# Performance work log

Measured on AMD Instinct MI355X. Metric: run time of the kernel, lower is better.

Reference implementation:

```python
import jax, jax.numpy as jnp
import numpy as np

B, L, D = 8, 2048, 1024
NH, M = 32, 16            # TTTConfig defaults: num_attention_heads=32, mini_batch_size=16
HD = D // NH              # 32
NM = L // M               # 128 mini-batches
DI = 2048                 # FFN hidden (configs.d_lower)
BASE_LR = 1.0
EPS = 1e-6


def setup_inputs() -> dict:
    key = jax.random.key(0)
    ks = jax.random.split(key, 12)
    n = lambda k, s, sc=0.02: jax.random.normal(k, s, jnp.float32) * sc
    return dict(
        enc_input=jax.random.normal(ks[0], (B, L, D), jnp.float32),
        ln0_g=jnp.ones((D,), jnp.float32), ln0_b=jnp.zeros((D,), jnp.float32),
        Wq=n(ks[1], (D, D)), Wk=n(ks[2], (D, D)), Wv=n(ks[3], (D, D)), Wo=n(ks[4], (D, D)),
        W1=n(ks[5], (NH, HD, HD)), b1=jnp.zeros((NH, 1, HD), jnp.float32),
        token_idx_delta=jnp.zeros((M,), jnp.float32),
        lr_w=n(ks[6], (NH, D)), lr_b=jnp.zeros((NH,), jnp.float32),
        ttt_ln_g=jnp.ones((NH, HD), jnp.float32), ttt_ln_b=jnp.zeros((NH, HD), jnp.float32),
        post_g=jnp.ones((D,), jnp.float32), post_b=jnp.zeros((D,), jnp.float32),
        ffn_g=jnp.ones((D,), jnp.float32), ffn_b=jnp.zeros((D,), jnp.float32),
        fw1=n(ks[7], (D, DI)), fb1=jnp.zeros((DI,), jnp.float32),
        fw2=n(ks[8], (DI, D)), fb2=jnp.zeros((D,), jnp.float32),
    )


def _layernorm(x, g, b):
    mu = x.mean(-1, keepdims=True)
    v = ((x - mu) ** 2).mean(-1, keepdims=True)
    return (x - mu) * jax.lax.rsqrt(v + EPS) * g + b


def _rope(x):
    # x: [B,NH,L,HD]; standard rotary embedding, theta=10000
    half = HD // 2
    inv = 1.0 / (10000.0 ** (jnp.arange(0, HD, 2, dtype=jnp.float32) / HD))
    pos = jnp.arange(L, dtype=jnp.float32)
    fr = pos[:, None] * inv[None, :]                    # [L, HD/2]
    emb = jnp.concatenate([fr, fr], -1)                 # [L, HD]
    cos, sin = jnp.cos(emb), jnp.sin(emb)
    rot = jnp.concatenate([-x[..., half:], x[..., :half]], -1)
    return x * cos + rot * sin


def reference(enc_input, ln0_g, ln0_b, Wq, Wk, Wv, Wo, W1, b1, token_idx_delta,
              lr_w, lr_b, ttt_ln_g, ttt_ln_b, post_g, post_b,
              ffn_g, ffn_b, fw1, fb1, fw2, fb2):
    residual = enc_input
    x = _layernorm(enc_input, ln0_g, ln0_b)

    def heads(t):  # [B,L,D] -> [B,NH,L,HD]
        return t.reshape(B, L, NH, HD).transpose(0, 2, 1, 3)

    XQ = _rope(heads(x @ Wq))
    XK = _rope(heads(x @ Wk))
    XV = heads(x @ Wv)

    # per-token learnable learning rates (sigmoid gate), token_idx schedule
    X_mb = x.reshape(B, NM, M, D)
    ttt_lr = jax.nn.sigmoid(jnp.einsum('bnkc,hc->bhnk', X_mb, lr_w) + lr_b[None, :, None, None])
    ttt_lr_eta = BASE_LR * ttt_lr / HD                               # [B,NH,NM,M]
    token_idx = jnp.clip(1.0 / jnp.arange(1, M + 1, dtype=jnp.float32) + token_idx_delta, 0.0, None)
    eta = token_idx[None, None, None, :, None] * ttt_lr_eta[:, :, :, None, :]  # [B,NH,NM,M,M]

    def to_scan(t):  # [B,NH,L,HD] -> [NM,B,NH,M,HD]
        return t.reshape(B, NH, NM, M, HD).transpose(2, 0, 1, 3, 4)

    xs = (to_scan(XQ), to_scan(XK), to_scan(XV), eta.transpose(2, 0, 1, 3, 4))

    lw = ttt_ln_g[:, None, :]   # [NH,1,HD]
    lb = ttt_ln_b[:, None, :]
    tril = jnp.tril(jnp.ones((M, M), jnp.float32))

    def ln_fwd(z):
        mu = z.mean(-1, keepdims=True)
        v = ((z - mu) ** 2).mean(-1, keepdims=True)
        return (z - mu) * jax.lax.rsqrt(v + EPS) * lw + lb

    def ln_l2_bwd(z, tgt):
        # gradient of 0.5*||LN(z)-tgt||^2 w.r.t. z (fused LN l2 backward)
        mu = z.mean(-1, keepdims=True)
        v = ((z - mu) ** 2).mean(-1, keepdims=True)
        std = jnp.sqrt(v + EPS)
        xhat = (z - mu) / std
        gxh = (xhat * lw + lb - tgt) * lw
        return (HD * gxh - gxh.sum(-1, keepdims=True)
                - xhat * (gxh * xhat).sum(-1, keepdims=True)) / (HD * std)

    W1_0 = jnp.broadcast_to(W1[None], (B, NH, HD, HD))
    b1_0 = jnp.broadcast_to(b1[None], (B, NH, 1, HD))

    def step(carry, inp):
        W, bvec = carry
        q, k, v_, e = inp                                    # [B,NH,M,HD], e: [B,NH,M,M]
        Z1 = k @ W + bvec
        grad = ln_l2_bwd(Z1, v_ - k)                         # [B,NH,M,HD]
        Attn1 = tril * (q @ k.transpose(0, 1, 3, 2))         # causal dual-form attention
        b_bar = bvec - (tril * e) @ grad
        Z1_bar = q @ W - (e * Attn1) @ grad + b_bar
        last_e = e[:, :, -1, :, None]                        # [B,NH,M,1]
        W_new = W - (last_e * k).transpose(0, 1, 3, 2) @ grad
        b_new = bvec - (last_e * grad).sum(-2, keepdims=True)
        return (W_new, b_new), q + ln_fwd(Z1_bar)

    _, outs = jax.lax.scan(step, (W1_0, b1_0), xs)           # [NM,B,NH,M,HD]
    out = outs.transpose(1, 0, 3, 2, 4).reshape(B, L, D)     # -> [B,L,D]
    out = _layernorm(out, post_g, post_b) @ Wo               # post_norm + o_proj
    out = out + residual                                     # dropout = identity (eval)

    # PositionWiseFeedForward (pre-LN, residual)
    r2 = out
    h = _layernorm(out, ffn_g, ffn_b)
    h = jax.nn.relu(h @ fw1 + fb1) @ fw2 + fb2
    return h + r2
```

## Files before the change

kernel.cpp:

```cpp
#include <hip/hip_runtime.h>
#include <hip/hip_bf16.h>
#include <stdint.h>

#define B_   8
#define L_   2048
#define D_   1024
#define NH_  32
#define M_   16
#define NM_  128
#define HD_  32
#define DI_  2048
#define BL_  16384
#define EPS_ 1e-6f

typedef __attribute__((ext_vector_type(8))) short  s16x8;
typedef __attribute__((ext_vector_type(4))) short  s16x4;
typedef __attribute__((ext_vector_type(8))) __bf16 bf16x8;
typedef __attribute__((ext_vector_type(4))) float  f32x4;
typedef __attribute__((ext_vector_type(4))) unsigned u32x4;

__device__ __forceinline__ float bf2f(short s){
  unsigned u = ((unsigned)(unsigned short)s) << 16;
  return __builtin_bit_cast(float, u);
}
__device__ __forceinline__ short f2bf(float f){
  unsigned u = __builtin_bit_cast(unsigned, f);
  u = u + 0x7FFFu + ((u >> 16) & 1u);
  return (short)(u >> 16);
}
__device__ __forceinline__ unsigned cvtpk(float lo, float hi){
  unsigned r;
  asm("v_cvt_pk_bf16_f32 %0, %1, %2" : "=v"(r) : "v"(lo), "v"(hi));
  return r;
}
template<int N>
__device__ __forceinline__ float ror_add(float v){
  const int y = __builtin_amdgcn_update_dpp(
      0, __builtin_bit_cast(int, v), 0x120 + N, 0xF, 0xF, true);
  return v + __builtin_bit_cast(float, y);
}
__device__ __forceinline__ float rsum16d(float v){
  v = ror_add<1>(v); v = ror_add<2>(v); v = ror_add<4>(v); v = ror_add<8>(v);
  return v;
}
__device__ __forceinline__ void wgbar(){
  asm volatile("s_waitcnt lgkmcnt(0)" ::: "memory");
  __builtin_amdgcn_s_barrier();
  __builtin_amdgcn_sched_barrier(0);
}
__device__ __forceinline__ void gl16(const void* g, void* l){
  __builtin_amdgcn_global_load_lds(
      (const __attribute__((address_space(1))) void*)g,
      (__attribute__((address_space(3))) void*)l, 16, 0, 0);
}

__global__ __launch_bounds__(256) void transpose_cast(
    const float* __restrict__ in, short* __restrict__ out, int R, int Cc)
{
  __shared__ float t[32][33];
  const int lx = threadIdx.x & 31, ly = threadIdx.x >> 5;
  const int r0 = blockIdx.y * 32, c0 = blockIdx.x * 32;
  #pragma unroll
  for (int s = 0; s < 4; ++s){
    const int r = ly + s*8;
    t[r][lx] = in[(size_t)(r0 + r)*Cc + c0 + lx];
  }
  __syncthreads();
  #pragma unroll
  for (int s = 0; s < 4; ++s){
    const int r = ly + s*8;
    out[(size_t)(c0 + r)*R + r0 + lx] = f2bf(t[lx][r]);
  }
}

struct TC4 { const float *s0,*s1,*s2,*s3; short *d0,*d1,*d2,*d3; };
__global__ __launch_bounds__(256) void transpose_cast4(TC4 p)
{
  __shared__ float t[32][33];
  const int z = blockIdx.z;
  const float* in = (z==0)?p.s0:(z==1)?p.s1:(z==2)?p.s2:p.s3;
  short* out      = (z==0)?p.d0:(z==1)?p.d1:(z==2)?p.d2:p.d3;
  const int lx = threadIdx.x & 31, ly = threadIdx.x >> 5;
  const int r0 = blockIdx.y * 32, c0 = blockIdx.x * 32;
  #pragma unroll
  for (int s = 0; s < 4; ++s){
    const int r = ly + s*8;
    t[r][lx] = in[(size_t)(r0 + r)*1024 + c0 + lx];
  }
  __syncthreads();
  #pragma unroll
  for (int s = 0; s < 4; ++s){
    const int r = ly + s*8;
    out[(size_t)(c0 + r)*1024 + r0 + lx] = f2bf(t[lx][r]);
  }
}

__global__ __launch_bounds__(256) void misc_prep(
    const float* __restrict__ lr_w, short* __restrict__ lrwb,
    float* __restrict__ ct, float* __restrict__ st)
{
  const int idx = blockIdx.x*256 + threadIdx.x;
  if (idx < NH_*D_){
    lrwb[idx] = f2bf(lr_w[idx]);
  } else {
    const int k = idx - NH_*D_;
    const int l = k >> 4, j = k & 15;
    const float inv = powf(10000.f, -(float)j * (1.f/16.f));
    const float fr  = (float)l * inv;
    ct[k] = cosf(fr);
    st[k] = sinf(fr);
  }
}

__global__ __launch_bounds__(256) void ln_rows(
    const float* __restrict__ in, const float* __restrict__ g,
    const float* __restrict__ bta, short* __restrict__ out)
{
  const int row = blockIdx.x, tid = threadIdx.x;
  const float4 v = ((const float4*)(in + (size_t)row*D_))[tid];
  float s  = v.x + v.y + v.z + v.w;
  float s2 = v.x*v.x + v.y*v.y + v.z*v.z + v.w*v.w;
  #pragma unroll
  for (int m = 1; m < 64; m <<= 1){ s += __shfl_xor(s, m); s2 += __shfl_xor(s2, m); }
  __shared__ float rs[4], rq[4];
  if ((tid & 63) == 0){ rs[tid>>6] = s; rq[tid>>6] = s2; }
  __syncthreads();
  s  = rs[0] + rs[1] + rs[2] + rs[3];
  s2 = rq[0] + rq[1] + rq[2] + rq[3];
  const float mu   = s  * (1.f/D_);
  const float var  = s2 * (1.f/D_) - mu*mu;
  const float rstd = rsqrtf(var + EPS_);
  const float4 gg = ((const float4*)g)[tid];
  const float4 bb = ((const float4*)bta)[tid];
  s16x4 o;
  o[0] = f2bf((v.x - mu)*rstd*gg.x + bb.x);
  o[1] = f2bf((v.y - mu)*rstd*gg.y + bb.y);
  o[2] = f2bf((v.z - mu)*rstd*gg.z + bb.z);
  o[3] = f2bf((v.w - mu)*rstd*gg.w + bb.w);
  ((s16x4*)(out + (size_t)row*D_))[tid] = o;
}

__global__ __launch_bounds__(256) void ln_rows_bf(
    const short* __restrict__ in, const float* __restrict__ g,
    const float* __restrict__ bta, short* __restrict__ out)
{
  const int row = blockIdx.x, tid = threadIdx.x;
  const s16x4 v4 = ((const s16x4*)(in + (size_t)row*D_))[tid];
  float v[4];
  #pragma unroll
  for (int e = 0; e < 4; ++e) v[e] = bf2f(v4[e]);
  float s  = v[0]+v[1]+v[2]+v[3];
  float s2 = v[0]*v[0]+v[1]*v[1]+v[2]*v[2]+v[3]*v[3];
  #pragma unroll
  for (int m = 1; m < 64; m <<= 1){ s += __shfl_xor(s, m); s2 += __shfl_xor(s2, m); }
  __shared__ float rs[4], rq[4];
  if ((tid & 63) == 0){ rs[tid>>6] = s; rq[tid>>6] = s2; }
  __syncthreads();
  s  = rs[0] + rs[1] + rs[2] + rs[3];
  s2 = rq[0] + rq[1] + rq[2] + rq[3];
  const float mu   = s  * (1.f/D_);
  const float var  = s2 * (1.f/D_) - mu*mu;
  const float rstd = rsqrtf(var + EPS_);
  const float4 gg = ((const float4*)g)[tid];
  const float4 bb = ((const float4*)bta)[tid];
  s16x4 o;
  #pragma unroll
  for (int e = 0; e < 4; ++e){
    const float gv = (e==0)?gg.x:(e==1)?gg.y:(e==2)?gg.z:gg.w;
    const float bv = (e==0)?bb.x:(e==1)?bb.y:(e==2)?bb.z:bb.w;
    o[e] = f2bf((v[e] - mu)*rstd*gv + bv);
  }
  ((s16x4*)(out + (size_t)row*D_))[tid] = o;
}

template<int ACT, int OUTBF, int BIAS, int RES, int RESB, int QKVOUT>
__global__ __launch_bounds__(512, 2) void gemm256(
    const short* __restrict__ A, const short* __restrict__ Bt,
    const float* __restrict__ bias, const float* __restrict__ res,
    const short* __restrict__ resb,
    float* __restrict__ Cf, short* __restrict__ Cb,
    const float* __restrict__ ct, const float* __restrict__ st,
    int Mr, int N, int K)
{
  __shared__ __align__(16) short As[4][8192];
  __shared__ __align__(16) short Bs[4][8192];
  const int tid  = threadIdx.x;
  const int lane = tid & 63, wid = tid >> 6;
  const int wr = wid >> 2, wc = wid & 3;
  const int nwg = gridDim.x * gridDim.y;
  const int wg  = blockIdx.y * gridDim.x + blockIdx.x;
  const int swz = (wg & 7) * (nwg >> 3) + (wg >> 3);
  const int bx  = swz % gridDim.x, by = swz / gridDim.x;
  const int row0 = by * 256, col0 = bx * 256;

  f32x4 acc[8][4] = {};

  const int kswz = (((tid & 3) ^ ((tid >> 3) & 3)) << 3);
  const short* gAb = A  + (size_t)(row0 + (tid >> 2)) * K + kswz;
  const short* gBb = Bt + (size_t)(col0 + (tid >> 2)) * K + kswz;
  short* lAb = &As[0][0] + tid*8;
  short* lBb = &Bs[0][0] + tid*8;

  auto stage = [&](int bt2, int t2){
    const size_t kb = (size_t)t2 * 32;
    gl16(gAb + kb,                   lAb + bt2*8192);
    gl16(gAb + kb + 128*(size_t)K,   lAb + bt2*8192 + 4096);
    gl16(gBb + kb,                   lBb + bt2*8192);
    gl16(gBb + kb + 128*(size_t)K,   lBb + bt2*8192 + 4096);
  };

  const int fr = lane & 15;
  const int k0 = (((lane >> 4) ^ ((lane >> 1) & 3)) << 3);

  const int nK = K >> 5;
  stage(0, 0); stage(1, 1); stage(2, 2);
  asm volatile("s_waitcnt vmcnt(8)" ::: "memory");
  __builtin_amdgcn_s_barrier();

  for (int kt = 0; kt < nK; ++kt){
    const int bt = kt & 3;
    const short* Ab = &As[0][0] + bt*8192 + wr*4096;
    const short* Bb = &Bs[0][0] + bt*8192 + (wc >> 1)*4096 + (wc & 1)*2048;
    bf16x8 af[8], bfv[4];
    #pragma unroll
    for (int m = 0; m < 8; ++m)
      af[m] = *(const bf16x8*)(Ab + (m*16 + fr)*32 + k0);
    #pragma unroll
    for (int n = 0; n < 4; ++n)
      bfv[n] = *(const bf16x8*)(Bb + (n*16 + fr)*32 + k0);
    if (kt + 3 < nK) stage((kt + 3) & 3, kt + 3);
    __builtin_amdgcn_s_setprio(1);
    #pragma unroll
    for (int m = 0; m < 8; ++m)
      #pragma unroll
      for (int n = 0; n < 4; ++n)
        acc[m][n] = __builtin_amdgcn_mfma_f32_16x16x32_bf16(af[m], bfv[n], acc[m][n], 0,0,0);
    __builtin_amdgcn_s_setprio(0);
    if (kt + 3 < nK)      asm volatile("s_waitcnt vmcnt(8)" ::: "memory");
    else if (kt + 2 < nK) asm volatile("s_waitcnt vmcnt(4)" ::: "memory");
    else if (kt + 1 < nK) asm volatile("s_waitcnt vmcnt(0)" ::: "memory");
    __builtin_amdgcn_s_barrier();
  }

  const int cr = (lane >> 4) * 4, cc = lane & 15;
  if (QKVOUT){
    const int part = col0 >> 10;
    #pragma unroll
    for (int m = 0; m < 8; ++m){
      const int gr0 = row0 + wr*128 + m*16 + cr;
      const int bidx = gr0 >> 11, l0 = gr0 & (L_-1);
      const int nn = l0 >> 4;
      if (part < 2){
        #pragma unroll
        for (int np = 0; np < 2; ++np){
          const int gc = col0 + wc*64 + np*32 + cc;
          const int hh = (gc & 1023) >> 5;
          short* tile = Cb + ((size_t)(bidx*NH_ + hh)*NM_ + nn)*2048;
          s16x4 r0v, r1v;
          #pragma unroll
          for (int r = 0; r < 4; ++r){
            const int l = l0 + r;
            const float cv = ct[l*16 + cc], sv = st[l*16 + cc];
            const float x0 = acc[m][np*2][r], x1 = acc[m][np*2+1][r];
            const short q0 = f2bf(x0*cv - x1*sv);
            const short q1 = f2bf(x1*cv + x0*sv);
            tile[part*512 + (cr + r)*32 + cc]      = q0;
            tile[part*512 + (cr + r)*32 + cc + 16] = q1;
            r0v[r] = q0; r1v[r] = q1;
          }
          if (part == 1){
            *(s16x4*)(tile + 1024 + cc*16 + cr)      = r0v;
            *(s16x4*)(tile + 1024 + (cc+16)*16 + cr) = r1v;
          }
        }
      } else {
        #pragma unroll
        for (int n = 0; n < 4; ++n){
          const int gc = col0 + wc*64 + n*16 + cc;
          const int hh = (gc & 1023) >> 5, dd = gc & 31;
          short* tile = Cb + ((size_t)(bidx*NH_ + hh)*NM_ + nn)*2048;
          s16x4 p;
          #pragma unroll
          for (int r = 0; r < 4; ++r) p[r] = f2bf(acc[m][n][r]);
          *(s16x4*)(tile + 1536 + dd*16 + cr) = p;
        }
      }
    }
    return;
  }
  #pragma unroll
  for (int m = 0; m < 8; ++m){
    #pragma unroll
    for (int n = 0; n < 4; ++n){
      const int gc = col0 + wc*64 + n*16 + cc;
      float bv = 0.f;
      if (BIAS) bv = bias[gc];
      #pragma unroll
      for (int r = 0; r < 4; ++r){
        const int gr = row0 + wr*128 + m*16 + cr + r;
        float v = acc[m][n][r] + bv;
        if (RES)  v += res[(size_t)gr*N + gc];
        if (RESB) v += bf2f(resb[(size_t)gr*N + gc]);
        if (ACT == 1) v = fmaxf(v, 0.f);
        if (OUTBF) Cb[(size_t)gr*N + gc] = f2bf(v);
        else       Cf[(size_t)gr*N + gc] = v;
      }
    }
  }
}

__global__ __launch_bounds__(256) void eta_kernel(
    const short* __restrict__ xb, const short* __restrict__ lrwb,
    const float* __restrict__ lr_b, float* __restrict__ eta)
{
  __shared__ __align__(16) short wl[NH_*1032];
  const int tid = threadIdx.x;
  const int lane = tid & 63, wv = tid >> 6;
  const int li = lane & 15, lh = lane >> 4;
  #pragma unroll
  for (int s = 0; s < 16; ++s){
    const int e = tid + 256*s;
    const int hrow = e >> 7, c = (e & 127) * 8;
    *(s16x8*)(wl + hrow*1032 + c) = ((const s16x8*)lrwb)[e];
  }
  __syncthreads();

  const int t0 = (blockIdx.x*4 + wv) * 16;
  const short* xrow = xb + (size_t)(t0 + li)*1024 + 8*lh;
  const short* w0p = wl + li*1032 + 8*lh;
  const short* w1p = wl + (16 + li)*1032 + 8*lh;
  f32x4 acc0 = {}, acc1 = {};
  #pragma unroll 4
  for (int s = 0; s < 32; ++s){
    const bf16x8 a  = *(const bf16x8*)(xrow + s*32);
    const bf16x8 b0 = *(const bf16x8*)(w0p + s*32);
    const bf16x8 b1 = *(const bf16x8*)(w1p + s*32);
    acc0 = __builtin_amdgcn_mfma_f32_16x16x32_bf16(a, b0, acc0, 0,0,0);
    acc1 = __builtin_amdgcn_mfma_f32_16x16x32_bf16(a, b1, acc1, 0,0,0);
  }
  const int t = t0 + 4*lh;
  const int bidx = t >> 11, l = t & (L_-1), n = l >> 4, im = l & 15;
  float* e0 = eta + ((size_t)(bidx*NH_ + li)*NM_ + n)*M_ + im;
  float* e1 = eta + ((size_t)(bidx*NH_ + 16 + li)*NM_ + n)*M_ + im;
  const float lb0 = lr_b[li], lb1 = lr_b[16 + li];
  #pragma unroll
  for (int r = 0; r < 4; ++r){
    e0[r] = 1.f/(1.f + __expf(-(acc0[r] + lb0))) * (1.f/32.f);
    e1[r] = 1.f/(1.f + __expf(-(acc1[r] + lb1))) * (1.f/32.f);
  }
}

__global__ __launch_bounds__(192) void scan_kernel(
    const short* __restrict__ Q5, const float* __restrict__ eta,
    const float* __restrict__ W1, const float* __restrict__ b1,
    const float* __restrict__ tdelta, const float* __restrict__ lng,
    const float* __restrict__ lnb, short* __restrict__ out)
{
  const int bh = blockIdx.x;
  const int h = bh & 31, b = bh >> 5;
  const int lane = threadIdx.x & 63;
  const int wv = threadIdx.x >> 6;
  const int li = lane & 15, lh = lane >> 4;

  __shared__ __align__(16) short WTl[2][32*40];
  __shared__ __align__(16) short GTl[2][32*24];
  __shared__ float BBl[2][2][16];
  __shared__ __align__(16) float AT[16*20];
  __shared__ __align__(16) short QLl[2][16*40];

  const short* chain = Q5 + (size_t)bh * (NM_*2048);
  const float* ech   = eta + (size_t)bh * (NM_*16);

  float lw[2], lbv[2];
  #pragma unroll
  for (int hh = 0; hh < 2; ++hh){
    lw[hh]  = lng[h*32 + 16*hh + li];
    lbv[hh] = lnb[h*32 + 16*hh + li];
  }

  if (wv == 0){
    f32x4 Wq[2][2];
    #pragma unroll
    for (int rb = 0; rb < 2; ++rb)
      #pragma unroll
      for (int cb = 0; cb < 2; ++cb)
        #pragma unroll
        for (int r = 0; r < 4; ++r)
          Wq[rb][cb][r] = W1[h*1024 + (16*rb + 4*lh + r)*32 + 16*cb + li];
    float bb[2];
    bb[0] = b1[h*32 + li];  bb[1] = b1[h*32 + 16 + li];
    const float lef = fmaxf(1.f/16.f + tdelta[15], 0.f);

    auto writeWT = [&](int sl){
      #pragma unroll
      for (int cb = 0; cb < 2; ++cb)
        #pragma unroll
        for (int rb = 0; rb < 2; ++rb){
          const unsigned p0 = cvtpk(Wq[rb][cb][0], Wq[rb][cb][1]);
          const unsigned p1 = cvtpk(Wq[rb][cb][2], Wq[rb][cb][3]);
          *(uint64_t*)(&WTl[sl][0] + (16*cb + li)*40 + 16*rb + 4*lh) =
              ((uint64_t)p1 << 32) | p0;
        }
    };
    auto readWf = [&](int sl, bf16x8* Wf){
      Wf[0] = *(const bf16x8*)(&WTl[sl][0] + li*40 + 8*lh);
      Wf[1] = *(const bf16x8*)(&WTl[sl][0] + (16 + li)*40 + 8*lh);
    };

    writeWT(0);
    if (lh == 0){ BBl[0][0][li] = bb[0]; BBl[0][1][li] = bb[1]; }
    bf16x8 Wf[2];
    readWf(0, Wf);

    struct P0 { s16x8 kA, kTq0, kTq1; s16x4 kTe0, kTe1, vTe0, vTe1;
                f32x4 lr0, lr1, lr2, lr3; };
    auto ld0 = [&](int n) -> P0 {
      const short* t = chain + (size_t)n*2048;
      const float* e = ech + n*16;
      P0 p;
      p.kA   = *(const s16x8*)(t + 512 + li*32 + 8*lh);
      p.kTq0 = *(const s16x8*)(t + 1024 + li*16 + 8*(lh & 1));
      p.kTq1 = *(const s16x8*)(t + 1024 + (16 + li)*16 + 8*(lh & 1));
      p.kTe0 = *(const s16x4*)(t + 1024 + li*16 + 4*lh);
      p.kTe1 = *(const s16x4*)(t + 1024 + (16 + li)*16 + 4*lh);
      p.vTe0 = *(const s16x4*)(t + 1536 + li*16 + 4*lh);
      p.vTe1 = *(const s16x4*)(t + 1536 + (16 + li)*16 + 4*lh);
      p.lr0 = *(const f32x4*)(e);     p.lr1 = *(const f32x4*)(e + 4);
      p.lr2 = *(const f32x4*)(e + 8); p.lr3 = *(const f32x4*)(e + 12);
      return p;
    };

    P0 cur = ld0(0);
    wgbar();

    const int gcol = (8*lh) & 15;
    #pragma unroll 1
    for (int p = 0; p <= NM_; ++p){
      if (p < NM_){
        const int n = p;
        const int sl = n & 1;
        P0 nxt = ld0(n + 1 < NM_ ? n + 1 : NM_ - 1);
        const bf16x8 kAf = __builtin_bit_cast(bf16x8, cur.kA);

        f32x4 zac[2];
        #pragma unroll
        for (int hh = 0; hh < 2; ++hh){
          f32x4 c0; c0[0]=bb[hh]; c0[1]=bb[hh]; c0[2]=bb[hh]; c0[3]=bb[hh];
          zac[hh] = __builtin_amdgcn_mfma_f32_16x16x32_bf16(kAf, Wf[hh], c0, 0,0,0);
        }

        float xh[2][4], grad[2][4], rstdv[4];
        #pragma unroll
        for (int r = 0; r < 4; ++r){
          float s  = rsum16d(zac[0][r] + zac[1][r]);
          float q2 = rsum16d(zac[0][r]*zac[0][r] + zac[1][r]*zac[1][r]);
          const float mu  = s * (1.f/32.f);
          const float var = q2 * (1.f/32.f) - mu*mu;
          const float rstd = rsqrtf(var + EPS_);
          rstdv[r] = rstd;
          xh[0][r] = (zac[0][r] - mu) * rstd;
          xh[1][r] = (zac[1][r] - mu) * rstd;
        }
        #pragma unroll
        for (int r = 0; r < 4; ++r){
          const float t0 = bf2f(cur.vTe0[r]) - bf2f(cur.kTe0[r]);
          const float t1 = bf2f(cur.vTe1[r]) - bf2f(cur.kTe1[r]);
          const float g0 = (xh[0][r]*lw[0] + lbv[0] - t0)*lw[0];
          const float g1 = (xh[1][r]*lw[1] + lbv[1] - t1)*lw[1];
          const float sg  = rsum16d(g0 + g1);
          const float sgx = rsum16d(g0*xh[0][r] + g1*xh[1][r]);
          const float f = rstdv[r] * (1.f/32.f);
          grad[0][r] = (32.f*g0 - sg - xh[0][r]*sgx) * f;
          grad[1][r] = (32.f*g1 - sg - xh[1][r]*sgx) * f;
        }

        #pragma unroll
        for (int hh = 0; hh < 2; ++hh){
          const unsigned p0 = cvtpk(grad[hh][0], grad[hh][1]);
          const unsigned p1 = cvtpk(grad[hh][2], grad[hh][3]);
          *(uint64_t*)(&GTl[sl][0] + (16*hh + li)*24 + 4*lh) =
              ((uint64_t)p1 << 32) | p0;
        }
        bf16x8 gf[2];
        gf[0] = *(const bf16x8*)(&GTl[sl][0] + li*24 + gcol);
        gf[1] = *(const bf16x8*)(&GTl[sl][0] + (16 + li)*24 + gcol);

        const f32x4 plA = (lh & 1) ? cur.lr2 : cur.lr0;
        const f32x4 plB = (lh & 1) ? cur.lr3 : cur.lr1;
        #pragma unroll
        for (int rb = 0; rb < 2; ++rb){
          const s16x8 kq = rb ? cur.kTq1 : cur.kTq0;
          float av8[8];
          #pragma unroll
          for (int jj = 0; jj < 8; ++jj){
            const float lrv = (jj < 4) ? plA[jj] : plB[jj - 4];
            av8[jj] = (lh < 2) ? -lef * lrv * bf2f(kq[jj]) : 0.f;
          }
          u32x4 auv;
          auv[0] = cvtpk(av8[0], av8[1]); auv[1] = cvtpk(av8[2], av8[3]);
          auv[2] = cvtpk(av8[4], av8[5]); auv[3] = cvtpk(av8[6], av8[7]);
          const bf16x8 af = __builtin_bit_cast(bf16x8, auv);
          #pragma unroll
          for (int cb = 0; cb < 2; ++cb)
            Wq[rb][cb] = __builtin_amdgcn_mfma_f32_16x16x32_bf16(af, gf[cb], Wq[rb][cb], 0,0,0);
        }

        writeWT(sl ^ 1);
        readWf(sl ^ 1, Wf);

        f32x4 lrq;
        { const f32x4 t0 = (lh & 1) ? cur.lr1 : cur.lr0;
          const f32x4 t1 = (lh & 1) ? cur.lr3 : cur.lr2;
          lrq = (lh & 2) ? t1 : t0; }
        #pragma unroll
        for (int hh = 0; hh < 2; ++hh){
          float t = 0.f;
          #pragma unroll
          for (int r = 0; r < 4; ++r) t += lrq[r]*grad[hh][r];
          t += __shfl_xor(t, 16); t += __shfl_xor(t, 32);
          bb[hh] -= lef * t;
        }
        if (lh == 0){ BBl[sl ^ 1][0][li] = bb[0]; BBl[sl ^ 1][1][li] = bb[1]; }
        cur = nxt;
      }
      wgbar();
    }
  } else {
    const int par = wv - 1;
    const float tok_i = fmaxf(1.f/(float)(li+1) + tdelta[li], 0.f);
    short* outp = out + (size_t)b*L_*D_ + h*32;
    const int gcol = (8*lh) & 15;

    struct P1 { s16x8 qA, kA; f32x4 lr0, lr1, lr2, lr3; };
    auto ld1 = [&](int n) -> P1 {
      const short* t = chain + (size_t)n*2048;
      const float* e = ech + n*16;
      P1 p;
      p.qA = *(const s16x8*)(t + li*32 + 8*lh);
      p.kA = *(const s16x8*)(t + 512 + li*32 + 8*lh);
      p.lr0 = *(const f32x4*)(e);     p.lr1 = *(const f32x4*)(e + 4);
      p.lr2 = *(const f32x4*)(e + 8); p.lr3 = *(const f32x4*)(e + 12);
      return p;
    };

    auto outln = [&](int n, const f32x4* yac){
      #pragma unroll
      for (int r = 0; r < 4; ++r){
        const float s  = rsum16d(yac[0][r] + yac[1][r]);
        const float q2 = rsum16d(yac[0][r]*yac[0][r] + yac[1][r]*yac[1][r]);
        const float mu   = s * (1.f/32.f);
        const float var  = q2 * (1.f/32.f) - mu*mu;
        const float rstd = rsqrtf(var + EPS_);
        const int row = 4*lh + r;
        #pragma unroll
        for (int hh = 0; hh < 2; ++hh){
          const float qv = bf2f(QLl[n & 1][row*40 + 16*hh + li]);
          const float o  = qv + (yac[hh][r] - mu)*rstd*lw[hh] + lbv[hh];
          outp[(size_t)(n*16 + row)*D_ + 16*hh + li] = f2bf(o);
        }
      }
    };

    P1 cur = ld1(par);
    wgbar();

    f32x4 ycur[2] = {};
    bf16x8 pCur = {};
    #pragma unroll 1
    for (int p = 0; p <= NM_; ++p){
      if (p >= 1 && ((p - 1) & 1) == par){
        const int m = p - 1;
        const int sl = m & 1;
        bf16x8 gf0 = *(const bf16x8*)(&GTl[sl][0] + li*24 + gcol);
        bf16x8 gf1 = *(const bf16x8*)(&GTl[sl][0] + (16 + li)*24 + gcol);
        ycur[0] = __builtin_amdgcn_mfma_f32_16x16x32_bf16(pCur, gf0, ycur[0], 0,0,0);
        ycur[1] = __builtin_amdgcn_mfma_f32_16x16x32_bf16(pCur, gf1, ycur[1], 0,0,0);
        outln(m, ycur);
      }
      if (p < NM_ && (p & 1) == par){
        const int sl = p & 1;
        bf16x8 Wf0 = *(const bf16x8*)(&WTl[sl][0] + li*40 + 8*lh);
        bf16x8 Wf1 = *(const bf16x8*)(&WTl[sl][0] + (16 + li)*40 + 8*lh);
        const float bb0 = BBl[sl][0][li];
        const float bb1 = BBl[sl][1][li];

        P1 nxt = ld1(p + 2 < NM_ ? p + 2 : p);
        const bf16x8 qAf = __builtin_bit_cast(bf16x8, cur.qA);
        const bf16x8 kAf = __builtin_bit_cast(bf16x8, cur.kA);

        *(s16x8*)(&QLl[sl][0] + li*40 + 8*lh) = cur.qA;

        f32x4 aac = {};
        aac = __builtin_amdgcn_mfma_f32_16x16x32_bf16(qAf, kAf, aac, 0,0,0);
        #pragma unroll
        for (int r = 0; r < 4; ++r)
          AT[(4*lh + r)*20 + li] = aac[r];

        f32x4 arA = {}, arB = {};
        if (lh < 2){
          arA = *(const f32x4*)(AT + li*20 + 8*lh);
          arB = *(const f32x4*)(AT + li*20 + 8*lh + 4);
        }
        const f32x4 plA = (lh & 1) ? cur.lr2 : cur.lr0;
        const f32x4 plB = (lh & 1) ? cur.lr3 : cur.lr1;
        float pv[8];
        #pragma unroll
        for (int jj = 0; jj < 8; ++jj){
          const float av  = (jj < 4) ? arA[jj] : arB[jj - 4];
          const float lrv = (jj < 4) ? plA[jj] : plB[jj - 4];
          const bool ok = (lh < 2) && (8*lh + jj <= li);
          pv[jj] = ok ? -tok_i * lrv * (1.f + av) : 0.f;
        }
        u32x4 ppv;
        ppv[0] = cvtpk(pv[0], pv[1]); ppv[1] = cvtpk(pv[2], pv[3]);
        ppv[2] = cvtpk(pv[4], pv[5]); ppv[3] = cvtpk(pv[6], pv[7]);
        pCur = __builtin_bit_cast(bf16x8, ppv);

        { f32x4 c0; c0[0]=bb0; c0[1]=bb0; c0[2]=bb0; c0[3]=bb0;
          ycur[0] = __builtin_amdgcn_mfma_f32_16x16x32_bf16(qAf, Wf0, c0, 0,0,0); }
        { f32x4 c0; c0[0]=bb1; c0[1]=bb1; c0[2]=bb1; c0[3]=bb1;
          ycur[1] = __builtin_amdgcn_mfma_f32_16x16x32_bf16(qAf, Wf1, c0, 0,0,0); }

        cur = nxt;
      }
      wgbar();
    }
  }
}

extern "C" void kernel_launch(void* const* d_in, const int* in_sizes, int n_in,
                              void* d_out, int out_size, void* d_ws, size_t ws_size,
                              hipStream_t stream)
{
  const float* enc    = (const float*)d_in[0];
  const float* ln0_g  = (const float*)d_in[1];
  const float* ln0_b  = (const float*)d_in[2];
  const float* Wq     = (const float*)d_in[3];
  const float* Wk     = (const float*)d_in[4];
  const float* Wv     = (const float*)d_in[5];
  const float* Wo     = (const float*)d_in[6];
  const float* W1     = (const float*)d_in[7];
  const float* b1     = (const float*)d_in[8];
  const float* tdelta = (const float*)d_in[9];
  const float* lr_w   = (const float*)d_in[10];
  const float* lr_b   = (const float*)d_in[11];
  const float* ttt_g  = (const float*)d_in[12];
  const float* ttt_b  = (const float*)d_in[13];
  const float* post_g = (const float*)d_in[14];
  const float* post_b = (const float*)d_in[15];
  const float* ffn_g  = (const float*)d_in[16];
  const float* ffn_b  = (const float*)d_in[17];
  const float* fw1    = (const float*)d_in[18];
  const float* fb1    = (const float*)d_in[19];
  const float* fw2    = (const float*)d_in[20];
  const float* fb2    = (const float*)d_in[21];

  char* ws = (char*)d_ws;
  short* Q5    = (short*)(ws + 0);
  short* XB    = (short*)(ws + 134217728);
  short* SCANB = (short*)(ws + 134217728);
  short* WQKVT = (short*)(ws + 167772160);
  short* WOT   = (short*)(ws + 174063616);
  short* FW1T  = (short*)(ws + 176160768);
  short* FW2T  = (short*)(ws + 180355072);
  short* LRWB  = (short*)(ws + 184549376);
  float* CT    = (float*)(ws + 184614912);
  float* ST    = (float*)(ws + 184745984);
  float* ETA   = (float*)(ws + 184877056);
  short* YB    = (short*)(ws + 0);
  short* HB    = (short*)(ws + 33554432);
  short* T1    = (short*)(ws + 67108864);
  short* R2B   = (short*)(ws + 134217728);
  float* R2    = (float*)d_out;

  dim3 b256(256), b512(512);
  TC4 tc;
  tc.s0 = Wq; tc.s1 = Wk; tc.s2 = Wv; tc.s3 = Wo;
  tc.d0 = WQKVT; tc.d1 = WQKVT + 1048576; tc.d2 = WQKVT + 2097152; tc.d3 = WOT;
  transpose_cast4<<<dim3(32,32,4), b256, 0, stream>>>(tc);
  transpose_cast<<<dim3(64,32), b256, 0, stream>>>(fw1, FW1T, D_, DI_);
  transpose_cast<<<dim3(32,64), b256, 0, stream>>>(fw2, FW2T, DI_, D_);
  misc_prep<<<dim3(256), b256, 0, stream>>>(lr_w, LRWB, CT, ST);

  ln_rows<<<BL_, b256, 0, stream>>>(enc, ln0_g, ln0_b, XB);
  gemm256<0,0,0,0,0,1><<<dim3(12,64), b512, 0, stream>>>(XB, WQKVT, nullptr, nullptr, nullptr,
                                                         nullptr, Q5, CT, ST, BL_, 3072, D_);
  eta_kernel<<<dim3(256), b256, 0, stream>>>(XB, LRWB, lr_b, ETA);
  scan_kernel<<<dim3(256), dim3(192), 0, stream>>>(Q5, ETA, W1, b1, tdelta,
                                                   ttt_g, ttt_b, SCANB);
  ln_rows_bf<<<BL_, b256, 0, stream>>>(SCANB, post_g, post_b, YB);
  gemm256<0,1,0,1,0,0><<<dim3(4,64), b512, 0, stream>>>(YB, WOT, nullptr, enc, nullptr,
                                                        nullptr, R2B, nullptr, nullptr, BL_, D_, D_);
  ln_rows_bf<<<BL_, b256, 0, stream>>>(R2B, ffn_g, ffn_b, HB);
  gemm256<1,1,1,0,0,0><<<dim3(8,64), b512, 0, stream>>>(HB, FW1T, fb1, nullptr, nullptr,
                                                        nullptr, T1, nullptr, nullptr, BL_, DI_, D_);
  gemm256<0,0,1,0,1,0><<<dim3(4,64), b512, 0, stream>>>(T1, FW2T, fb2, nullptr, R2B,
                                                        R2, nullptr, nullptr, nullptr, BL_, D_, DI_);
}
```

Before: 504.8 us.

## Use 16x16x16 MFMA with register-resident operands to drop LDS transposes in scan

The weight update and the output correction now use 16x16x16 bf16 MFMAs, called through inline asm, whose K=16 operand layout matches the accumulator layout already held in registers. Gradients are packed straight from registers into a lane-indexed LDS buffer, replacing the transposed GTl layout. The attention matrix is computed transposed so each lane already holds its P row, which removes the AT LDS round trip and the kTq loads. The goal is to shorten the serial per-mini-batch critical path by removing LDS writes, reads and barriers, at the cost of fixed s_nop padding and asm volatile blocks the compiler cannot schedule around.

```diff
diff --git a/kernel.cpp b/kernel.cpp
--- a/kernel.cpp
+++ b/kernel.cpp
@@ -18,6 +18,7 @@
 typedef __attribute__((ext_vector_type(8))) __bf16 bf16x8;
 typedef __attribute__((ext_vector_type(4))) float  f32x4;
 typedef __attribute__((ext_vector_type(4))) unsigned u32x4;
+typedef __attribute__((ext_vector_type(2))) unsigned u32x2;
 
 __device__ __forceinline__ float bf2f(short s){
   unsigned u = ((unsigned)(unsigned short)s) << 16;
@@ -32,6 +33,16 @@
   unsigned r;
   asm("v_cvt_pk_bf16_f32 %0, %1, %2" : "=v"(r) : "v"(lo), "v"(hi));
   return r;
+}
+__device__ __forceinline__ void mfma16x2(s16x4 a, s16x4 b0, s16x4 b1,
+                                         f32x4& c0, f32x4& c1){
+  asm volatile(
+      "s_nop 1\n\t"
+      "v_mfma_f32_16x16x16_bf16 %0, %2, %3, %0\n\t"
+      "v_mfma_f32_16x16x16_bf16 %1, %2, %4, %1\n\t"
+      "s_nop 7\n\t"
+      "s_nop 3"
+      : "+v"(c0), "+v"(c1) : "v"(a), "v"(b0), "v"(b1));
 }
 template<int N>
 __device__ __forceinline__ float ror_add(float v){
@@ -363,9 +374,8 @@
   const int li = lane & 15, lh = lane >> 4;
 
   __shared__ __align__(16) short WTl[2][32*40];
-  __shared__ __align__(16) short GTl[2][32*24];
+  __shared__ __align__(16) unsigned PGl[2][256];
   __shared__ float BBl[2][2][16];
-  __shared__ __align__(16) float AT[16*20];
   __shared__ __align__(16) short QLl[2][16*40];
 
   const short* chain = Q5 + (size_t)bh * (NM_*2048);
@@ -412,15 +422,13 @@
     bf16x8 Wf[2];
     readWf(0, Wf);
 
-    struct P0 { s16x8 kA, kTq0, kTq1; s16x4 kTe0, kTe1, vTe0, vTe1;
+    struct P0 { s16x8 kA; s16x4 kTe0, kTe1, vTe0, vTe1;
                 f32x4 lr0, lr1, lr2, lr3; };
     auto ld0 = [&](int n) -> P0 {
       const short* t = chain + (size_t)n*2048;
       const float* e = ech + n*16;
       P0 p;
       p.kA   = *(const s16x8*)(t + 512 + li*32 + 8*lh);
-      p.kTq0 = *(const s16x8*)(t + 1024 + li*16 + 8*(lh & 1));
-      p.kTq1 = *(const s16x8*)(t + 1024 + (16 + li)*16 + 8*(lh & 1));
       p.kTe0 = *(const s16x4*)(t + 1024 + li*16 + 4*lh);
       p.kTe1 = *(const s16x4*)(t + 1024 + (16 + li)*16 + 4*lh);
       p.vTe0 = *(const s16x4*)(t + 1536 + li*16 + 4*lh);
@@ -433,7 +441,6 @@
     P0 cur = ld0(0);
     wgbar();
 
-    const int gcol = (8*lh) & 15;
     #pragma unroll 1
     for (int p = 0; p <= NM_; ++p){
       if (p < NM_){
@@ -474,44 +481,35 @@
           grad[1][r] = (32.f*g1 - sg - xh[1][r]*sgx) * f;
         }
 
-        #pragma unroll
-        for (int hh = 0; hh < 2; ++hh){
-          const unsigned p0 = cvtpk(grad[hh][0], grad[hh][1]);
-          const unsigned p1 = cvtpk(grad[hh][2], grad[hh][3]);
-          *(uint64_t*)(&GTl[sl][0] + (16*hh + li)*24 + 4*lh) =
-              ((uint64_t)p1 << 32) | p0;
-        }
-        bf16x8 gf[2];
-        gf[0] = *(const bf16x8*)(&GTl[sl][0] + li*24 + gcol);
-        gf[1] = *(const bf16x8*)(&GTl[sl][0] + (16 + li)*24 + gcol);
-
-        const f32x4 plA = (lh & 1) ? cur.lr2 : cur.lr0;
-        const f32x4 plB = (lh & 1) ? cur.lr3 : cur.lr1;
-        #pragma unroll
-        for (int rb = 0; rb < 2; ++rb){
-          const s16x8 kq = rb ? cur.kTq1 : cur.kTq0;
-          float av8[8];
-          #pragma unroll
-          for (int jj = 0; jj < 8; ++jj){
-            const float lrv = (jj < 4) ? plA[jj] : plB[jj - 4];
-            av8[jj] = (lh < 2) ? -lef * lrv * bf2f(kq[jj]) : 0.f;
-          }
-          u32x4 auv;
-          auv[0] = cvtpk(av8[0], av8[1]); auv[1] = cvtpk(av8[2], av8[3]);
-          auv[2] = cvtpk(av8[4], av8[5]); auv[3] = cvtpk(av8[6], av8[7]);
-          const bf16x8 af = __builtin_bit_cast(bf16x8, auv);
-          #pragma unroll
-          for (int cb = 0; cb < 2; ++cb)
-            Wq[rb][cb] = __builtin_amdgcn_mfma_f32_16x16x32_bf16(af, gf[cb], Wq[rb][cb], 0,0,0);
-        }
-
-        writeWT(sl ^ 1);
-        readWf(sl ^ 1, Wf);
+        const unsigned g00 = cvtpk(grad[0][0], grad[0][1]);
+        const unsigned g01 = cvtpk(grad[0][2], grad[0][3]);
+        const unsigned g10 = cvtpk(grad[1][0], grad[1][1]);
+        const unsigned g11 = cvtpk(grad[1][2], grad[1][3]);
+        u32x4 gq; gq[0]=g00; gq[1]=g01; gq[2]=g10; gq[3]=g11;
+        *(u32x4*)&PGl[sl][lane*4] = gq;
+        u32x2 tg0; tg0[0]=g00; tg0[1]=g01;
+        u32x2 tg1; tg1[0]=g10; tg1[1]=g11;
+        const s16x4 gB0 = __builtin_bit_cast(s16x4, tg0);
+        const s16x4 gB1 = __builtin_bit_cast(s16x4, tg1);
 
         f32x4 lrq;
         { const f32x4 t0 = (lh & 1) ? cur.lr1 : cur.lr0;
           const f32x4 t1 = (lh & 1) ? cur.lr3 : cur.lr2;
           lrq = (lh & 2) ? t1 : t0; }
+
+        #pragma unroll
+        for (int rb = 0; rb < 2; ++rb){
+          const s16x4 kq = rb ? cur.kTe1 : cur.kTe0;
+          const unsigned a0 = cvtpk(-lef*lrq[0]*bf2f(kq[0]), -lef*lrq[1]*bf2f(kq[1]));
+          const unsigned a1 = cvtpk(-lef*lrq[2]*bf2f(kq[2]), -lef*lrq[3]*bf2f(kq[3]));
+          u32x2 ta; ta[0]=a0; ta[1]=a1;
+          const s16x4 afq = __builtin_bit_cast(s16x4, ta);
+          mfma16x2(afq, gB0, gB1, Wq[rb][0], Wq[rb][1]);
+        }
+
+        writeWT(sl ^ 1);
+        readWf(sl ^ 1, Wf);
+
         #pragma unroll
         for (int hh = 0; hh < 2; ++hh){
           float t = 0.f;
@@ -529,7 +527,6 @@
     const int par = wv - 1;
     const float tok_i = fmaxf(1.f/(float)(li+1) + tdelta[li], 0.f);
     short* outp = out + (size_t)b*L_*D_ + h*32;
-    const int gcol = (8*lh) & 15;
 
     struct P1 { s16x8 qA, kA; f32x4 lr0, lr1, lr2, lr3; };
     auto ld1 = [&](int n) -> P1 {
@@ -565,16 +562,18 @@
     wgbar();
 
     f32x4 ycur[2] = {};
-    bf16x8 pCur = {};
+    s16x4 pCur4 = {};
     #pragma unroll 1
     for (int p = 0; p <= NM_; ++p){
       if (p >= 1 && ((p - 1) & 1) == par){
         const int m = p - 1;
         const int sl = m & 1;
-        bf16x8 gf0 = *(const bf16x8*)(&GTl[sl][0] + li*24 + gcol);
-        bf16x8 gf1 = *(const bf16x8*)(&GTl[sl][0] + (16 + li)*24 + gcol);
-        ycur[0] = __builtin_amdgcn_mfma_f32_16x16x32_bf16(pCur, gf0, ycur[0], 0,0,0);
-        ycur[1] = __builtin_amdgcn_mfma_f32_16x16x32_bf16(pCur, gf1, ycur[1], 0,0,0);
+        const u32x4 gq = *(const u32x4*)&PGl[sl][lane*4];
+        u32x2 tg0; tg0[0]=gq[0]; tg0[1]=gq[1];
+        u32x2 tg1; tg1[0]=gq[2]; tg1[1]=gq[3];
+        const s16x4 gB0 = __builtin_bit_cast(s16x4, tg0);
+        const s16x4 gB1 = __builtin_bit_cast(s16x4, tg1);
+        mfma16x2(pCur4, gB0, gB1, ycur[0], ycur[1]);
         outln(m, ycur);
       }
       if (p < NM_ && (p & 1) == par){
@@ -590,31 +589,22 @@
 
         *(s16x8*)(&QLl[sl][0] + li*40 + 8*lh) = cur.qA;
 
-        f32x4 aac = {};
-        aac = __builtin_amdgcn_mfma_f32_16x16x32_bf16(qAf, kAf, aac, 0,0,0);
-        #pragma unroll
-        for (int r = 0; r < 4; ++r)
-          AT[(4*lh + r)*20 + li] = aac[r];
-
-        f32x4 arA = {}, arB = {};
-        if (lh < 2){
-          arA = *(const f32x4*)(AT + li*20 + 8*lh);
-          arB = *(const f32x4*)(AT + li*20 + 8*lh + 4);
-        }
-        const f32x4 plA = (lh & 1) ? cur.lr2 : cur.lr0;
-        const f32x4 plB = (lh & 1) ? cur.lr3 : cur.lr1;
-        float pv[8];
-        #pragma unroll
-        for (int jj = 0; jj < 8; ++jj){
-          const float av  = (jj < 4) ? arA[jj] : arB[jj - 4];
-          const float lrv = (jj < 4) ? plA[jj] : plB[jj - 4];
-          const bool ok = (lh < 2) && (8*lh + jj <= li);
-          pv[jj] = ok ? -tok_i * lrv * (1.f + av) : 0.f;
-        }
-        u32x4 ppv;
-        ppv[0] = cvtpk(pv[0], pv[1]); ppv[1] = cvtpk(pv[2], pv[3]);
-        ppv[2] = cvtpk(pv[4], pv[5]); ppv[3] = cvtpk(pv[6], pv[7]);
-        pCur = __builtin_bit_cast(bf16x8, ppv);
+        f32x4 zz = {};
+        const f32x4 aacT = __builtin_amdgcn_mfma_f32_16x16x32_bf16(kAf, qAf, zz, 0,0,0);
+
+        f32x4 lrq;
+        { const f32x4 t0 = (lh & 1) ? cur.lr1 : cur.lr0;
+          const f32x4 t1 = (lh & 1) ? cur.lr3 : cur.lr2;
+          lrq = (lh & 2) ? t1 : t0; }
+
+        float pv[4];
+        #pragma unroll
+        for (int e = 0; e < 4; ++e){
+          const bool ok = (4*lh + e <= li);
+          pv[e] = ok ? -tok_i * lrq[e] * (1.f + aacT[e]) : 0.f;
+        }
+        u32x2 tp; tp[0] = cvtpk(pv[0], pv[1]); tp[1] = cvtpk(pv[2], pv[3]);
+        pCur4 = __builtin_bit_cast(s16x4, tp);
 
         { f32x4 c0; c0[0]=bb0; c0[1]=bb0; c0[2]=bb0; c0[3]=bb0;
           ycur[0] = __builtin_amdgcn_mfma_f32_16x16x32_bf16(qAf, Wf0, c0, 0,0,0); }
```

New measurement: 507.9 us. Within noise of the previous version (+0.6%).
